# Performance work log

Hardware: AMD Instinct MI355X
Metric: run time of the kernel (lower is better)

## Reference

```python
import jax, jax.numpy as jnp
import numpy as np

D_MODEL = 1024
NUM_HEADS = 16
D_K = D_MODEL // NUM_HEADS  # 64
THETA = 10000.0
B = 2
L = 2048


def _rope(x, positions):
    # x: [B, H, L, d_k], positions: [B, L]
    half = D_K // 2
    freqs = 1.0 / (THETA ** (jnp.arange(0, D_K, 2, dtype=jnp.float32) / D_K))  # [half]
    angles = positions.astype(jnp.float32)[..., None] * freqs  # [B, L, half]
    cos = jnp.cos(angles)[:, None, :, :]  # [B, 1, L, half]
    sin = jnp.sin(angles)[:, None, :, :]
    x_even = x[..., 0::2]
    x_odd = x[..., 1::2]
    r_even = x_even * cos - x_odd * sin
    r_odd = x_even * sin + x_odd * cos
    # interleave back: [..., half, 2] -> [..., d_k]
    return jnp.stack([r_even, r_odd], axis=-1).reshape(x.shape)


def setup_inputs() -> dict:
    key = jax.random.key(0)
    ks = jax.random.split(key, 5)
    std = np.sqrt(2.0 / (D_MODEL + D_MODEL))
    x = jax.random.normal(ks[0], (B, L, D_MODEL), dtype=jnp.float32)
    token_positions = jnp.broadcast_to(jnp.arange(L, dtype=jnp.int64 if jax.config.jax_enable_x64 else jnp.int32), (B, L))
    WQ = jax.random.truncated_normal(ks[1], -3.0, 3.0, (D_MODEL, D_MODEL), dtype=jnp.float32) * std
    WK = jax.random.truncated_normal(ks[2], -3.0, 3.0, (D_MODEL, D_MODEL), dtype=jnp.float32) * std
    WV = jax.random.truncated_normal(ks[3], -3.0, 3.0, (D_MODEL, D_MODEL), dtype=jnp.float32) * std
    WO = jax.random.truncated_normal(ks[4], -3.0, 3.0, (D_MODEL, D_MODEL), dtype=jnp.float32) * std
    return {"x": x, "token_positions": token_positions, "WQ": WQ, "WK": WK, "WV": WV, "WO": WO}


def reference(x, token_positions, WQ, WK, WV, WO):
    # Projections: W is [out, in] -> y = x @ W.T
    Q = jnp.einsum('bld,ed->ble', x, WQ)
    K = jnp.einsum('bld,ed->ble', x, WK)
    V = jnp.einsum('bld,ed->ble', x, WV)
    # [B, L, H*d] -> [B, H, L, d]
    def split_heads(t):
        return t.reshape(B, L, NUM_HEADS, D_K).transpose(0, 2, 1, 3)
    Q, K, V = split_heads(Q), split_heads(K), split_heads(V)
    Q = _rope(Q, token_positions)
    K = _rope(K, token_positions)
    scores = jnp.einsum('bhqd,bhkd->bhqk', Q, K) / np.sqrt(D_K).astype(np.float32)
    causal = jnp.tril(jnp.ones((L, L), dtype=bool))
    scores = jnp.where(causal, scores, -jnp.inf)
    attn = jax.nn.softmax(scores, axis=-1)
    out = jnp.einsum('bhqk,bhkd->bhqd', attn, V)  # [B, H, L, d]
    out = out.transpose(0, 2, 1, 3).reshape(B, L, D_MODEL)
    return jnp.einsum('bld,ed->ble', out, WO)
```

## Files before the change

kernel.cpp:

```cpp
#include <hip/hip_runtime.h>
#include <cstdint>
#include <cstddef>

#define D_MODEL 1024
#define NHEAD   16
#define DKH     64
#define BATCH   2
#define SEQ     2048
#define BL      (BATCH*SEQ)

typedef unsigned short u16;
typedef unsigned int   u32;
typedef __bf16 bf16_t;
typedef bf16_t bf16x8 __attribute__((ext_vector_type(8)));
typedef u16    u16x8  __attribute__((ext_vector_type(8)));
typedef u32    u32x4  __attribute__((ext_vector_type(4)));
typedef float  f32x4  __attribute__((ext_vector_type(4)));
typedef float  f32x16 __attribute__((ext_vector_type(16)));

__device__ __forceinline__ u16 f2bf(float f) {
  u32 u = __builtin_bit_cast(u32, f);
  u32 r = (u + 0x7FFFu + ((u >> 16) & 1u)) >> 16;
  return (u16)r;
}
__device__ __forceinline__ float bf2f(u16 h) {
  u32 u = ((u32)h) << 16;
  return __builtin_bit_cast(float, u);
}
__device__ __forceinline__ bf16x8 ldb8(const u16* p) {
  return __builtin_bit_cast(bf16x8, *(const u16x8*)p);
}
__device__ __forceinline__ void gl_lds16(const u16* g, u16* l) {
  __builtin_amdgcn_global_load_lds((const __attribute__((address_space(1))) void*)g,
                                   (__attribute__((address_space(3))) void*)l, 16, 0, 0);
}
#define MFMA16x16x32(a,b,c) __builtin_amdgcn_mfma_f32_16x16x32_bf16((a),(b),(c),0,0,0)
#define MFMA32x32x16(a,b,c) __builtin_amdgcn_mfma_f32_32x32x16_bf16((a),(b),(c),0,0,0)

__global__ void __launch_bounds__(256) cvt1_kernel(const float* __restrict__ in, u16* __restrict__ out, int n8) {
  int i = blockIdx.x * 256 + threadIdx.x;
  if (i >= n8) return;
  float4 a = ((const float4*)in)[2*i];
  float4 b = ((const float4*)in)[2*i+1];
  u16x8 o;
  o[0]=f2bf(a.x); o[1]=f2bf(a.y); o[2]=f2bf(a.z); o[3]=f2bf(a.w);
  o[4]=f2bf(b.x); o[5]=f2bf(b.y); o[6]=f2bf(b.z); o[7]=f2bf(b.w);
  ((u16x8*)out)[i] = o;
}

__global__ void __launch_bounds__(256) cvt4_kernel(const float* __restrict__ i0, const float* __restrict__ i1,
                                                   const float* __restrict__ i2, const float* __restrict__ i3,
                                                   u16* __restrict__ o0, u16* __restrict__ o1,
                                                   u16* __restrict__ o2, u16* __restrict__ o3, int n8) {
  int i = blockIdx.x * 256 + threadIdx.x;
  if (i >= n8) return;
  const float* in = (blockIdx.y == 0) ? i0 : (blockIdx.y == 1) ? i1 : (blockIdx.y == 2) ? i2 : i3;
  u16*        out = (blockIdx.y == 0) ? o0 : (blockIdx.y == 1) ? o1 : (blockIdx.y == 2) ? o2 : o3;
  float4 a = ((const float4*)in)[2*i];
  float4 b = ((const float4*)in)[2*i+1];
  u16x8 o;
  o[0]=f2bf(a.x); o[1]=f2bf(a.y); o[2]=f2bf(a.z); o[3]=f2bf(a.w);
  o[4]=f2bf(b.x); o[5]=f2bf(b.y); o[6]=f2bf(b.z); o[7]=f2bf(b.w);
  ((u16x8*)out)[i] = o;
}

__global__ void __launch_bounds__(256) rope_tab_kernel(float2* __restrict__ tab) {
  int t = blockIdx.x * 256 + threadIdx.x;
  int p = t >> 5, i = t & 31;
  float fr = exp2f(-(float)i * 0.41524101186092f);
  float sv, cv;
  __sincosf((float)p * fr, &sv, &cv);
  tab[t] = make_float2(cv, sv);
}

__global__ void __launch_bounds__(512, 2) gemm_qkv_kernel(const u16* __restrict__ A,
    const u16* __restrict__ Wq, const u16* __restrict__ Wk, const u16* __restrict__ Wv,
    u16* __restrict__ Qo, u16* __restrict__ Ko, u16* __restrict__ Vo,
    const int* __restrict__ pos, const float2* __restrict__ tab) {
  const u16* W = (blockIdx.z == 0) ? Wq : (blockIdx.z == 1) ? Wk : Wv;
  u16*       C = (blockIdx.z == 0) ? Qo : (blockIdx.z == 1) ? Ko : Vo;
  const int mode = (blockIdx.z == 0) ? 1 : (blockIdx.z == 1) ? 2 : 0;
  const int M = BL, N = D_MODEL, K = D_MODEL;

  __shared__ u16 Als[2][256*64];
  __shared__ u16 Bls[2][256*64];
  const int tid = threadIdx.x, lane = tid & 63, w = tid >> 6;
  const int wr = w >> 2, wc = w & 3;
  const int lr = lane & 15, lg = lane >> 4;
  const int m0 = blockIdx.x * 256, n0 = blockIdx.y * 256;
  f32x4 acc[8][4] = {};
  const int srow = lane >> 3;
  const int scol = (lane & 7) * 8;
  #pragma unroll
  for (int c = 0; c < 4; ++c) {
    const int rb = w*32 + c*8;
    gl_lds16(A + (size_t)(m0 + rb + srow)*K + scol, &Als[0][rb*64]);
    gl_lds16(W + (size_t)(n0 + rb + srow)*K + scol, &Bls[0][rb*64]);
  }
  __syncthreads();
  for (int k0 = 0; k0 < K; k0 += 64) {
    const int cur = (k0 >> 6) & 1, nxt = cur ^ 1;
    if (k0 + 64 < K) {
      #pragma unroll
      for (int c = 0; c < 4; ++c) {
        const int rb = w*32 + c*8;
        gl_lds16(A + (size_t)(m0 + rb + srow)*K + k0 + 64 + scol, &Als[nxt][rb*64]);
        gl_lds16(W + (size_t)(n0 + rb + srow)*K + k0 + 64 + scol, &Bls[nxt][rb*64]);
      }
    }
    #pragma unroll
    for (int ks = 0; ks < 2; ++ks) {
      bf16x8 am[8], bn[4];
      #pragma unroll
      for (int f = 0; f < 8; ++f)
        am[f] = ldb8(&Als[cur][(wr*128 + f*16 + lr)*64 + ks*32 + lg*8]);
      #pragma unroll
      for (int f = 0; f < 4; ++f)
        bn[f] = ldb8(&Bls[cur][(wc*64 + f*16 + lr)*64 + ks*32 + lg*8]);
      #pragma unroll
      for (int fm = 0; fm < 8; ++fm)
        #pragma unroll
        for (int fn = 0; fn < 4; ++fn)
          acc[fm][fn] = MFMA16x16x32(am[fm], bn[fn], acc[fm][fn]);
    }
    __syncthreads();
  }
  if (mode) {
    const float QS  = 0.18033688011112042f;
    const float sgn = (lane & 1) ? 1.0f : -1.0f;
    #pragma unroll
    for (int fm = 0; fm < 8; ++fm)
      #pragma unroll
      for (int r = 0; r < 4; ++r) {
        const int row = m0 + wr*128 + fm*16 + lg*4 + r;
        const int p = pos[row];
        #pragma unroll
        for (int fn = 0; fn < 4; ++fn) {
          const float2 cs = tab[p*32 + fn*8 + (lr >> 1)];
          float v  = acc[fm][fn][r];
          float vp = __shfl_xor(v, 1, 64);
          float out = v*cs.x + sgn*vp*cs.y;
          if (mode == 1) out *= QS;
          C[(size_t)row*N + n0 + wc*64 + fn*16 + lr] = f2bf(out);
        }
      }
  } else {
    #pragma unroll
    for (int fm = 0; fm < 8; ++fm)
      #pragma unroll
      for (int fn = 0; fn < 4; ++fn)
        #pragma unroll
        for (int r = 0; r < 4; ++r) {
          const int row = m0 + wr*128 + fm*16 + lg*4 + r;
          const int col = n0 + wc*64 + fn*16 + lr;
          C[(size_t)row*N + col] = f2bf(acc[fm][fn][r]);
        }
  }
}

__global__ void __launch_bounds__(256) gemm_out_kernel(const u16* __restrict__ A, const u16* __restrict__ W,
                                                       float* __restrict__ C) {
  const int M = BL, N = D_MODEL, K = D_MODEL;
  __shared__ u16 Als[2][128*64];
  __shared__ u16 Bls[2][128*64];
  const int tid = threadIdx.x, lane = tid & 63, w = tid >> 6;
  const int wr = w >> 1, wc = w & 1;
  const int lr = lane & 15, lg = lane >> 4;
  const int m0 = blockIdx.x * 128, n0 = blockIdx.y * 128;
  f32x4 acc[4][4] = {};
  const int srow = lane >> 3;
  const int scol = (lane & 7) * 8;
  #pragma unroll
  for (int c = 0; c < 4; ++c) {
    const int rb = w*32 + c*8;
    gl_lds16(A + (size_t)(m0 + rb + srow)*K + scol, &Als[0][rb*64]);
    gl_lds16(W + (size_t)(n0 + rb + srow)*K + scol, &Bls[0][rb*64]);
  }
  __syncthreads();
  for (int k0 = 0; k0 < K; k0 += 64) {
    const int cur = (k0 >> 6) & 1, nxt = cur ^ 1;
    if (k0 + 64 < K) {
      #pragma unroll
      for (int c = 0; c < 4; ++c) {
        const int rb = w*32 + c*8;
        gl_lds16(A + (size_t)(m0 + rb + srow)*K + k0 + 64 + scol, &Als[nxt][rb*64]);
        gl_lds16(W + (size_t)(n0 + rb + srow)*K + k0 + 64 + scol, &Bls[nxt][rb*64]);
      }
    }
    #pragma unroll
    for (int ks = 0; ks < 2; ++ks) {
      bf16x8 am[4], bn[4];
      #pragma unroll
      for (int f = 0; f < 4; ++f) {
        am[f] = ldb8(&Als[cur][(wr*64 + f*16 + lr)*64 + ks*32 + lg*8]);
        bn[f] = ldb8(&Bls[cur][(wc*64 + f*16 + lr)*64 + ks*32 + lg*8]);
      }
      #pragma unroll
      for (int fm = 0; fm < 4; ++fm)
        #pragma unroll
        for (int fn = 0; fn < 4; ++fn)
          acc[fm][fn] = MFMA16x16x32(am[fm], bn[fn], acc[fm][fn]);
    }
    __syncthreads();
  }
  #pragma unroll
  for (int fm = 0; fm < 4; ++fm)
    #pragma unroll
    for (int fn = 0; fn < 4; ++fn)
      #pragma unroll
      for (int r = 0; r < 4; ++r) {
        const int row = m0 + wr*64 + fm*16 + lg*4 + r;
        const int col = n0 + wc*64 + fn*16 + lr;
        C[(size_t)row*N + col] = acc[fm][fn][r];
      }
}

struct AttnLds {
  union {
    struct { u16 K[2][2][64*64]; u16 V[2][2][64*64]; } s;
    float mg[4*64*34];
  } u;
};

__device__ __forceinline__ void attn_pass(
    const int q0, const int T,
    const u16* __restrict__ Qb, const u16* __restrict__ Kb,
    const u16* __restrict__ Vb, u16* __restrict__ Ob,
    AttnLds& sh, const int lane, const int w)
{
  const int wl = w & 3, isB = w >> 2;
  const int l31 = lane & 31, h32 = lane >> 5;
  const int SPLIT = T >> 1;
  const int qw0 = q0 + wl * 32;
  const int srow  = lane >> 3;
  const int scol8 = ((lane & 7) ^ srow) * 8;
  const int t0 = isB ? SPLIT : 0;
  const int vswz = (l31 & 7) << 3;

  bf16x8 qf[4];
  #pragma unroll
  for (int kc = 0; kc < 4; ++kc)
    qf[kc] = ldb8(Qb + (size_t)(qw0 + l31)*D_MODEL + kc*16 + h32*8);
  f32x16 o0 = {}, o1 = {};
  float mrun = 0.0f, lrun = 0.0f;

  {
    const int kv = t0 * 64;
    #pragma unroll
    for (int c = 0; c < 2; ++c) {
      const int rb = wl*16 + c*8;
      gl_lds16(Kb + (size_t)(kv + rb + srow)*D_MODEL + scol8, &sh.u.s.K[isB][0][rb*64]);
    }
    u16x8 a = *(const u16x8*)(Vb + (size_t)(kv + lane)*D_MODEL + (wl*2)*8);
    u16x8 c = *(const u16x8*)(Vb + (size_t)(kv + lane)*D_MODEL + (wl*2+1)*8);
    #pragma unroll
    for (int j = 0; j < 8; ++j) sh.u.s.V[isB][0][(wl*16 + j)*64 + (lane ^ (j<<3))] = a[j];
    #pragma unroll
    for (int j = 0; j < 8; ++j) sh.u.s.V[isB][0][(wl*16 + 8 + j)*64 + (lane ^ (j<<3))] = c[j];
  }
  __syncthreads();

  for (int i = 0; i < SPLIT; ++i) {
    const int buf = i & 1, nbuf = buf ^ 1;
    const bool pf = (i + 1 < SPLIT);
    u16x8 vr0, vr1;
    if (pf) {
      const int kvn = (t0 + i + 1) * 64;
      #pragma unroll
      for (int c = 0; c < 2; ++c) {
        const int rb = wl*16 + c*8;
        gl_lds16(Kb + (size_t)(kvn + rb + srow)*D_MODEL + scol8, &sh.u.s.K[isB][nbuf][rb*64]);
      }
      vr0 = *(const u16x8*)(Vb + (size_t)(kvn + lane)*D_MODEL + (wl*2)*8);
      vr1 = *(const u16x8*)(Vb + (size_t)(kvn + lane)*D_MODEL + (wl*2+1)*8);
    }
    const int kv0 = (t0 + i) * 64;
    if (kv0 <= qw0 + 31) {
      const u16* K0 = sh.u.s.K[isB][buf];
      const u16* V0 = sh.u.s.V[isB][buf];
      f32x16 s[2];
      #pragma unroll
      for (int r = 0; r < 16; ++r) { s[0][r] = -mrun; s[1][r] = -mrun; }
      #pragma unroll
      for (int kc = 0; kc < 4; ++kc) {
        const int sl = ((2*kc + h32) ^ (l31 & 7)) * 8;
        bf16x8 k0 = ldb8(&K0[(l31)*64 + sl]);
        bf16x8 k1 = ldb8(&K0[(32 + l31)*64 + sl]);
        s[0] = MFMA32x32x16(k0, qf[kc], s[0]);
        s[1] = MFMA32x32x16(k1, qf[kc], s[1]);
      }
      if (kv0 + 63 > qw0) {
        const int qrow = qw0 + l31;
        #pragma unroll
        for (int kb = 0; kb < 2; ++kb)
          #pragma unroll
          for (int r = 0; r < 16; ++r) {
            int kp = kv0 + kb*32 + (r&3) + 8*(r>>2) + 4*h32;
            if (kp > qrow) s[kb][r] = -1e30f;
          }
      }
      float t[16];
      #pragma unroll
      for (int j = 0; j < 16; ++j) t[j] = fmaxf(s[0][j], s[1][j]);
      #pragma unroll
      for (int st = 8; st >= 1; st >>= 1)
        #pragma unroll
        for (int j = 0; j < 16; ++j) if (j < st) t[j] = fmaxf(t[j], t[j + st]);
      float mx = t[0];
      mx = fmaxf(mx, __shfl_xor(mx, 32, 64));
      if (!__all(mx <= 8.0f)) {
        const float d  = fmaxf(mx, 0.0f);
        const float al = exp2f(-d);
        #pragma unroll
        for (int r = 0; r < 16; ++r) {
          float ar = __shfl(al, (r&3) + 8*(r>>2) + 4*h32, 64);
          o0[r] *= ar;
          o1[r] *= ar;
        }
        lrun *= al;
        mrun += d;
        #pragma unroll
        for (int kb = 0; kb < 2; ++kb)
          #pragma unroll
          for (int r = 0; r < 16; ++r) s[kb][r] -= d;
      }
      #pragma unroll
      for (int kb = 0; kb < 2; ++kb)
        #pragma unroll
        for (int r = 0; r < 16; ++r)
          s[kb][r] = exp2f(s[kb][r]);
      float us[16];
      #pragma unroll
      for (int j = 0; j < 16; ++j) us[j] = s[0][j] + s[1][j];
      #pragma unroll
      for (int st = 8; st >= 1; st >>= 1)
        #pragma unroll
        for (int j = 0; j < 16; ++j) if (j < st) us[j] += us[j + st];
      float ps = us[0];
      ps += __shfl_xor(ps, 32, 64);
      lrun += ps;
      #pragma unroll
      for (int kb = 0; kb < 2; ++kb) {
        u32 pk[8], sw[8];
        #pragma unroll
        for (int k2 = 0; k2 < 8; ++k2) {
          u32 pk_;
          float lo = s[kb][2*k2], hi = s[kb][2*k2+1];
          asm("v_cvt_pk_bf16_f32 %0, %1, %2" : "=v"(pk_) : "v"(lo), "v"(hi));
          pk[k2] = pk_;
          sw[k2] = (u32)__shfl_xor((int)pk_, 32, 64);
        }
        #pragma unroll
        for (int lm = 0; lm < 2; ++lm) {
          const int c = 2*kb + lm;
          u32x4 fw;
          fw[0] = h32 ? sw[4*lm+2] : pk[4*lm+0];
          fw[1] = h32 ? sw[4*lm+3] : pk[4*lm+1];
          fw[2] = h32 ? pk[4*lm+2] : sw[4*lm+0];
          fw[3] = h32 ? pk[4*lm+3] : sw[4*lm+1];
          bf16x8 pfr = __builtin_bit_cast(bf16x8, fw);
          bf16x8 v0 = ldb8(&V0[(l31)*64 + ((16*c + 8*h32) ^ vswz)]);
          bf16x8 v1 = ldb8(&V0[(32 + l31)*64 + ((16*c + 8*h32) ^ vswz)]);
          o0 = MFMA32x32x16(pfr, v0, o0);
          o1 = MFMA32x32x16(pfr, v1, o1);
        }
      }
    }
    if (pf) {
      u16* Vtn = sh.u.s.V[isB][nbuf];
      #pragma unroll
      for (int j = 0; j < 8; ++j) Vtn[(wl*16 + j)*64 + (lane ^ (j<<3))] = vr0[j];
      #pragma unroll
      for (int j = 0; j < 8; ++j) Vtn[(wl*16 + 8 + j)*64 + (lane ^ (j<<3))] = vr1[j];
    }
    __syncthreads();
  }
  float* mg = sh.u.mg;
  if (isB) {
    float* slot = mg + (size_t)(wl*64 + lane) * 34;
    #pragma unroll
    for (int r = 0; r < 16; ++r) { slot[r] = o0[r]; slot[16 + r] = o1[r]; }
    slot[32] = mrun; slot[33] = lrun;
  }
  __syncthreads();
  if (!isB) {
    const float* slot = mg + (size_t)(wl*64 + lane) * 34;
    const float mB = slot[32], lB = slot[33];
    const float m  = fmaxf(mrun, mB);
    const float eA = exp2f(mrun - m), eB = exp2f(mB - m);
    const float linv = 1.0f / (lrun * eA + lB * eB);
    #pragma unroll
    for (int r = 0; r < 16; ++r) {
      const int rp = (r&3) + 8*(r>>2) + 4*h32;
      const float eAr = __shfl(eA, rp, 64);
      const float eBr = __shfl(eB, rp, 64);
      const float lir = __shfl(linv, rp, 64);
      const float v0 = (o0[r]*eAr + slot[r]*eBr) * lir;
      const float v1 = (o1[r]*eAr + slot[16 + r]*eBr) * lir;
      const size_t grow = (size_t)(qw0 + rp) * D_MODEL;
      Ob[grow + l31]      = f2bf(v0);
      Ob[grow + 32 + l31] = f2bf(v1);
    }
  }
}

__global__ void __launch_bounds__(512) attn_kernel(const u16* __restrict__ Q, const u16* __restrict__ K,
                                                   const u16* __restrict__ V, u16* __restrict__ O) {
  __shared__ AttnLds sh;
  const int tid = threadIdx.x, lane = tid & 63, w = tid >> 6;
  const int n = blockIdx.x;
  const int bh = n & 31;
  const int q = 15 - (n >> 5);
  const int b = bh >> 4, head = bh & 15;
  const size_t headoff = (size_t)b * SEQ * D_MODEL + head * DKH;
  const u16* Qb = Q + headoff;
  const u16* Kb = K + headoff;
  const u16* Vb = V + headoff;
  u16* Ob = (u16*)O + headoff;
  attn_pass(q*128, 2*(q+1), Qb, Kb, Vb, Ob, sh, lane, w);
}

extern "C" void kernel_launch(void* const* d_in, const int* in_sizes, int n_in,
                              void* d_out, int out_size, void* d_ws, size_t ws_size,
                              hipStream_t stream) {
  const float* x  = (const float*)d_in[0];
  const int* pos  = (const int*)d_in[1];
  const float* WQ = (const float*)d_in[2];
  const float* WK = (const float*)d_in[3];
  const float* WV = (const float*)d_in[4];
  const float* WO = (const float*)d_in[5];
  u16* ws = (u16*)d_ws;
  const size_t NX = (size_t)BL * D_MODEL;
  const size_t NW = (size_t)D_MODEL * D_MODEL;
  u16* xb  = ws;
  u16* wqb = xb  + NX;
  u16* wkb = wqb + NW;
  u16* wvb = wkb + NW;
  u16* wob = wvb + NW;
  u16* qb  = wob + NW;
  u16* kb  = qb  + NX;
  u16* vb  = kb  + NX;
  u16* ab  = vb  + NX;
  float2* tab = (float2*)(ab + NX);

  rope_tab_kernel<<<dim3(SEQ*32/256), 256, 0, stream>>>(tab);
  cvt1_kernel<<<dim3((unsigned)(NX/8/256)), 256, 0, stream>>>(x, xb, (int)(NX/8));
  cvt4_kernel<<<dim3((unsigned)(NW/8/256), 4), 256, 0, stream>>>(WQ, WK, WV, WO, wqb, wkb, wvb, wob, (int)(NW/8));
  gemm_qkv_kernel<<<dim3(BL/256, D_MODEL/256, 3), 512, 0, stream>>>(xb, wqb, wkb, wvb, qb, kb, vb, pos, tab);
  attn_kernel<<<dim3(512), 512, 0, stream>>>(qb, kb, vb, ab);
  gemm_out_kernel<<<dim3(BL/128, D_MODEL/128), 256, 0, stream>>>(ab, wob, (float*)d_out);
}
```

Before: 143.5 us.

## Compute RoPE sin/cos inline in QKV epilogue and single-buffer output GEMM

Drops the separate rope table kernel and computes the rotation angles with exp2f and __sincosf directly in the QKV GEMM epilogue, which removes one launch and the table reads. The output projection GEMM also moves from double-buffered LDS with prefetch to a single buffer with a sync before and after each load. This halves its LDS footprint, possibly allowing more resident blocks, but it stops overlapping global loads with MFMA work. Fast sincos on large position values may lose some accuracy.

```diff
diff --git a/kernel.cpp b/kernel.cpp
--- a/kernel.cpp
+++ b/kernel.cpp
@@ -64,23 +64,14 @@
   ((u16x8*)out)[i] = o;
 }
 
-__global__ void __launch_bounds__(256) rope_tab_kernel(float2* __restrict__ tab) {
-  int t = blockIdx.x * 256 + threadIdx.x;
-  int p = t >> 5, i = t & 31;
-  float fr = exp2f(-(float)i * 0.41524101186092f);
-  float sv, cv;
-  __sincosf((float)p * fr, &sv, &cv);
-  tab[t] = make_float2(cv, sv);
-}
-
 __global__ void __launch_bounds__(512, 2) gemm_qkv_kernel(const u16* __restrict__ A,
     const u16* __restrict__ Wq, const u16* __restrict__ Wk, const u16* __restrict__ Wv,
     u16* __restrict__ Qo, u16* __restrict__ Ko, u16* __restrict__ Vo,
-    const int* __restrict__ pos, const float2* __restrict__ tab) {
+    const int* __restrict__ pos) {
   const u16* W = (blockIdx.z == 0) ? Wq : (blockIdx.z == 1) ? Wk : Wv;
   u16*       C = (blockIdx.z == 0) ? Qo : (blockIdx.z == 1) ? Ko : Vo;
   const int mode = (blockIdx.z == 0) ? 1 : (blockIdx.z == 1) ? 2 : 0;
-  const int M = BL, N = D_MODEL, K = D_MODEL;
+  const int N = D_MODEL, K = D_MODEL;
 
   __shared__ u16 Als[2][256*64];
   __shared__ u16 Bls[2][256*64];
@@ -128,18 +119,23 @@
   if (mode) {
     const float QS  = 0.18033688011112042f;
     const float sgn = (lane & 1) ? 1.0f : -1.0f;
+    float fr[4];
+    #pragma unroll
+    for (int fn = 0; fn < 4; ++fn)
+      fr[fn] = exp2f(-(float)((fn*16 + lr) >> 1) * 0.41524101186092f);
     #pragma unroll
     for (int fm = 0; fm < 8; ++fm)
       #pragma unroll
       for (int r = 0; r < 4; ++r) {
         const int row = m0 + wr*128 + fm*16 + lg*4 + r;
-        const int p = pos[row];
+        const float p = (float)pos[row];
         #pragma unroll
         for (int fn = 0; fn < 4; ++fn) {
-          const float2 cs = tab[p*32 + fn*8 + (lr >> 1)];
+          float sv, cv;
+          __sincosf(p * fr[fn], &sv, &cv);
           float v  = acc[fm][fn][r];
           float vp = __shfl_xor(v, 1, 64);
-          float out = v*cs.x + sgn*vp*cs.y;
+          float out = v*cv + sgn*vp*sv;
           if (mode == 1) out *= QS;
           C[(size_t)row*N + n0 + wc*64 + fn*16 + lr] = f2bf(out);
         }
@@ -160,9 +156,9 @@
 
 __global__ void __launch_bounds__(256) gemm_out_kernel(const u16* __restrict__ A, const u16* __restrict__ W,
                                                        float* __restrict__ C) {
-  const int M = BL, N = D_MODEL, K = D_MODEL;
-  __shared__ u16 Als[2][128*64];
-  __shared__ u16 Bls[2][128*64];
+  const int N = D_MODEL, K = D_MODEL;
+  __shared__ u16 Als[128*64];
+  __shared__ u16 Bls[128*64];
   const int tid = threadIdx.x, lane = tid & 63, w = tid >> 6;
   const int wr = w >> 1, wc = w & 1;
   const int lr = lane & 15, lg = lane >> 4;
@@ -170,30 +166,22 @@
   f32x4 acc[4][4] = {};
   const int srow = lane >> 3;
   const int scol = (lane & 7) * 8;
-  #pragma unroll
-  for (int c = 0; c < 4; ++c) {
-    const int rb = w*32 + c*8;
-    gl_lds16(A + (size_t)(m0 + rb + srow)*K + scol, &Als[0][rb*64]);
-    gl_lds16(W + (size_t)(n0 + rb + srow)*K + scol, &Bls[0][rb*64]);
-  }
-  __syncthreads();
   for (int k0 = 0; k0 < K; k0 += 64) {
-    const int cur = (k0 >> 6) & 1, nxt = cur ^ 1;
-    if (k0 + 64 < K) {
-      #pragma unroll
-      for (int c = 0; c < 4; ++c) {
-        const int rb = w*32 + c*8;
-        gl_lds16(A + (size_t)(m0 + rb + srow)*K + k0 + 64 + scol, &Als[nxt][rb*64]);
-        gl_lds16(W + (size_t)(n0 + rb + srow)*K + k0 + 64 + scol, &Bls[nxt][rb*64]);
-      }
-    }
+    __syncthreads();
+    #pragma unroll
+    for (int c = 0; c < 4; ++c) {
+      const int rb = w*32 + c*8;
+      gl_lds16(A + (size_t)(m0 + rb + srow)*K + k0 + scol, &Als[rb*64]);
+      gl_lds16(W + (size_t)(n0 + rb + srow)*K + k0 + scol, &Bls[rb*64]);
+    }
+    __syncthreads();
     #pragma unroll
     for (int ks = 0; ks < 2; ++ks) {
       bf16x8 am[4], bn[4];
       #pragma unroll
       for (int f = 0; f < 4; ++f) {
-        am[f] = ldb8(&Als[cur][(wr*64 + f*16 + lr)*64 + ks*32 + lg*8]);
-        bn[f] = ldb8(&Bls[cur][(wc*64 + f*16 + lr)*64 + ks*32 + lg*8]);
+        am[f] = ldb8(&Als[(wr*64 + f*16 + lr)*64 + ks*32 + lg*8]);
+        bn[f] = ldb8(&Bls[(wc*64 + f*16 + lr)*64 + ks*32 + lg*8]);
       }
       #pragma unroll
       for (int fm = 0; fm < 4; ++fm)
@@ -201,7 +189,6 @@
         for (int fn = 0; fn < 4; ++fn)
           acc[fm][fn] = MFMA16x16x32(am[fm], bn[fn], acc[fm][fn]);
     }
-    __syncthreads();
   }
   #pragma unroll
   for (int fm = 0; fm < 4; ++fm)
@@ -441,12 +428,10 @@
   u16* kb  = qb  + NX;
   u16* vb  = kb  + NX;
   u16* ab  = vb  + NX;
-  float2* tab = (float2*)(ab + NX);
-
-  rope_tab_kernel<<<dim3(SEQ*32/256), 256, 0, stream>>>(tab);
+
   cvt1_kernel<<<dim3((unsigned)(NX/8/256)), 256, 0, stream>>>(x, xb, (int)(NX/8));
   cvt4_kernel<<<dim3((unsigned)(NW/8/256), 4), 256, 0, stream>>>(WQ, WK, WV, WO, wqb, wkb, wvb, wob, (int)(NW/8));
-  gemm_qkv_kernel<<<dim3(BL/256, D_MODEL/256, 3), 512, 0, stream>>>(xb, wqb, wkb, wvb, qb, kb, vb, pos, tab);
+  gemm_qkv_kernel<<<dim3(BL/256, D_MODEL/256, 3), 512, 0, stream>>>(xb, wqb, wkb, wvb, qb, kb, vb, pos);
   attn_kernel<<<dim3(512), 512, 0, stream>>>(qb, kb, vb, ab);
   gemm_out_kernel<<<dim3(BL/128, D_MODEL/128), 256, 0, stream>>>(ab, wob, (float*)d_out);
 }
```

Measured after the change: 135.2 us. 5.8% less time.
